# Optimization experiments

Hardware: AMD Instinct MI355X
Metric: run time of the kernel (lower is better)

The kernel has to match this reference:

```python
import jax, jax.numpy as jnp
import numpy as np

B, F, D = 1024, 160000, 16


def setup_inputs() -> dict:
    key = jax.random.key(0)
    k1, k2, k3 = jax.random.split(key, 3)
    x = jax.random.randint(k1, (B, F), 0, 2, dtype=jnp.int32)  # multi-hot transaction
    emb_w = jax.random.normal(k2, (F, D), dtype=jnp.float32) * 0.05  # FM factor table
    bias_w = jax.random.normal(k3, (F, 1), dtype=jnp.float32) * 0.05  # per-field linear bias
    g_bias = jnp.zeros((), dtype=jnp.float32)  # global bias
    return {"x": x, "emb_w": emb_w, "bias_w": bias_w, "g_bias": g_bias}


def reference(x, emb_w, bias_w, g_bias):
    # mask[b,f] = 1 where field f is active (row > 0 in original tf code)
    mask = (x > 0).astype(emb_w.dtype)  # [B, F]
    # sum of active embeddings per row: equals gather+sum in the original
    ev = mask @ emb_w  # [B, D]
    # sum of squared norms of active embeddings per row
    rowsq = jnp.sum(emb_w * emb_w, axis=1)  # [F]
    sum_sq = mask @ rowsq  # [B]
    # 0.5 * (sum_{i,j} e_i . e_j - sum_i ||e_i||^2) == FM pairwise interaction
    second = 0.5 * (jnp.sum(ev * ev, axis=-1) - sum_sq)  # [B]
    # linear term: global bias + sum of active field biases
    linear = g_bias + mask @ bias_w  # [B, 1]
    return linear + second[:, None]  # [B, 1]
```

## Files before the change

kernel.cpp:

```cpp
#include <hip/hip_runtime.h>

#define B_ROWS 1024
#define F_FLD  160000
#define D_DIM  16
#define TCOLS  256
#define NCHUNK (F_FLD / TCOLS)
#define NSTAT  (D_DIM + 1)
#define ACC_N  (B_ROWS * NSTAT)
#define RED_SLAB 25

__global__ __launch_bounds__(256) void fm_prep(const float* __restrict__ emb,
                                               const float* __restrict__ bias,
                                               float* __restrict__ c,
                                               float* __restrict__ acc) {
    int i = blockIdx.x * 256 + threadIdx.x;
    if (i < F_FLD) {
        const float4* e = (const float4*)(emb + (size_t)i * D_DIM);
        float4 e0 = e[0], e1 = e[1], e2 = e[2], e3 = e[3];
        float s = e0.x*e0.x + e0.y*e0.y + e0.z*e0.z + e0.w*e0.w
                + e1.x*e1.x + e1.y*e1.y + e1.z*e1.z + e1.w*e1.w
                + e2.x*e2.x + e2.y*e2.y + e2.z*e2.z + e2.w*e2.w
                + e3.x*e3.x + e3.y*e3.y + e3.z*e3.z + e3.w*e3.w;
        c[i] = bias[i] - 0.5f * s;
    }
    if (i < ACC_N) acc[i] = 0.0f;
}

__global__ __launch_bounds__(256) void fm_main(const int* __restrict__ x,
                                               const float* __restrict__ emb,
                                               const float* __restrict__ c,
                                               float* __restrict__ partial,
                                               float* __restrict__ acc,
                                               int use_partial) {
    __shared__ unsigned long long msk[4][256];
    const int tid  = threadIdx.x;
    const int wave = tid >> 6;
    const int lane = tid & 63;
    const int rowbase = blockIdx.y * 256;
    const int c0 = blockIdx.x * TCOLS;

    {
        const int4* xp = (const int4*)(x + (size_t)(rowbase + wave * 64) * F_FLD + c0)
                         + lane;
        const size_t rstride = F_FLD / 4;
        for (int i = 0; i < 64; i += 8) {
            int4 v[8];
#pragma unroll
            for (int k = 0; k < 8; ++k) v[k] = xp[(size_t)(i + k) * rstride];
#pragma unroll
            for (int k = 0; k < 8; ++k) {
                unsigned long long m0 = __ballot(v[k].x > 0);
                unsigned long long m1 = __ballot(v[k].y > 0);
                unsigned long long m2 = __ballot(v[k].z > 0);
                unsigned long long m3 = __ballot(v[k].w > 0);
                if (lane == 0) {
                    int r = wave * 64 + i + k;
                    msk[0][r] = m0; msk[1][r] = m1; msk[2][r] = m2; msk[3][r] = m3;
                }
            }
        }
    }
    __syncthreads();

    unsigned long long m0 = msk[0][tid], m1 = msk[1][tid],
                       m2 = msk[2][tid], m3 = msk[3][tid];
    float ev[D_DIM];
#pragma unroll
    for (int d = 0; d < D_DIM; ++d) ev[d] = 0.0f;
    float cacc = 0.0f;

    const float* eb = emb + (size_t)c0 * D_DIM;
    const float* cb = c + c0;
#pragma unroll 4
    for (int l = 0; l < 64; ++l) {
#pragma unroll
        for (int j = 0; j < 4; ++j) {
            float mm = (((j == 0 ? m0 : j == 1 ? m1 : j == 2 ? m2 : m3) >> l) & 1ull)
                           ? 1.0f : 0.0f;
            const float4* e = (const float4*)(eb + (size_t)(4 * l + j) * D_DIM);
            float4 e0 = e[0], e1 = e[1], e2 = e[2], e3 = e[3];
            ev[0]  += mm * e0.x;  ev[1]  += mm * e0.y;
            ev[2]  += mm * e0.z;  ev[3]  += mm * e0.w;
            ev[4]  += mm * e1.x;  ev[5]  += mm * e1.y;
            ev[6]  += mm * e1.z;  ev[7]  += mm * e1.w;
            ev[8]  += mm * e2.x;  ev[9]  += mm * e2.y;
            ev[10] += mm * e2.z;  ev[11] += mm * e2.w;
            ev[12] += mm * e3.x;  ev[13] += mm * e3.y;
            ev[14] += mm * e3.z;  ev[15] += mm * e3.w;
            cacc   += mm * cb[4 * l + j];
        }
    }

    const int row = rowbase + tid;
    if (use_partial) {
        float* p = partial + (size_t)blockIdx.x * ACC_N + row;
#pragma unroll
        for (int d = 0; d < D_DIM; ++d) p[d * B_ROWS] = ev[d];
        p[D_DIM * B_ROWS] = cacc;
    } else {
#pragma unroll
        for (int d = 0; d < D_DIM; ++d) atomicAdd(acc + d * B_ROWS + row, ev[d]);
        atomicAdd(acc + D_DIM * B_ROWS + row, cacc);
    }
}

__global__ __launch_bounds__(256) void fm_reduce(const float* __restrict__ partial,
                                                 float* __restrict__ acc) {
    int t = blockIdx.x * 256 + threadIdx.x;
    if (t >= ACC_N) return;
    const float* p = partial + (size_t)blockIdx.y * RED_SLAB * ACC_N + t;
    float s = 0.0f;
#pragma unroll 5
    for (int k = 0; k < RED_SLAB; ++k) s += p[(size_t)k * ACC_N];
    atomicAdd(acc + t, s);
}

__global__ __launch_bounds__(256) void fm_final(const float* __restrict__ acc,
                                                const float* __restrict__ g_bias,
                                                float* __restrict__ out) {
    int row = blockIdx.x * 256 + threadIdx.x;
    if (row >= B_ROWS) return;
    float s = 0.0f;
#pragma unroll
    for (int d = 0; d < D_DIM; ++d) {
        float v = acc[d * B_ROWS + row];
        s += v * v;
    }
    out[row] = g_bias[0] + acc[D_DIM * B_ROWS + row] + 0.5f * s;
}

extern "C" void kernel_launch(void* const* d_in, const int* in_sizes, int n_in,
                              void* d_out, int out_size, void* d_ws, size_t ws_size,
                              hipStream_t stream) {
    const int*   x      = (const int*)d_in[0];
    const float* emb_w  = (const float*)d_in[1];
    const float* bias_w = (const float*)d_in[2];
    const float* g_bias = (const float*)d_in[3];
    float*       out    = (float*)d_out;

    size_t c_bytes   = (size_t)F_FLD * sizeof(float);
    size_t acc_bytes = (size_t)ACC_N * sizeof(float);
    size_t par_bytes = (size_t)NCHUNK * ACC_N * sizeof(float);
    float* c       = (float*)d_ws;
    float* acc     = (float*)((char*)d_ws + c_bytes);
    float* partial = (float*)((char*)d_ws + c_bytes + acc_bytes);
    int use_partial = (ws_size >= c_bytes + acc_bytes + par_bytes) ? 1 : 0;

    fm_prep<<<dim3((F_FLD + 255) / 256), dim3(256), 0, stream>>>(emb_w, bias_w, c, acc);
    fm_main<<<dim3(NCHUNK, B_ROWS / 256), dim3(256), 0, stream>>>(
        x, emb_w, c, partial, acc, use_partial);
    if (use_partial)
        fm_reduce<<<dim3((ACC_N + 255) / 256, NCHUNK / RED_SLAB), dim3(256), 0, stream>>>(
            partial, acc);
    fm_final<<<dim3((B_ROWS + 255) / 256), dim3(256), 0, stream>>>(acc, g_bias, out);
}
```

Measured before the change: 930.0 us.

## Compute masked embedding sums with bf16 MFMA instead of scalar FMA loops

Replaces the per-thread scalar loop over 256 fields with bf16 16x16x32 MFMA instructions. Ballot bitmasks are expanded into bf16 0/1 A-fragments, and a new pack kernel converts the embedding table and the combined bias/square-norm vector into bf16 B-fragment layout. Partials and accumulators move to a row-major [row][17] layout to match the MFMA output. This is meant to remove the ALU-bound FMA work, which costs far more than streaming x. In exchange it adds an extra pack pass, drops the block barrier before the mask reads, and rounds the embeddings and c terms to bf16, which risks accuracy.

```diff
diff --git a/kernel.cpp b/kernel.cpp
--- a/kernel.cpp
+++ b/kernel.cpp
@@ -1,13 +1,32 @@
 #include <hip/hip_runtime.h>
+#include <hip/hip_bf16.h>
 
 #define B_ROWS 1024
 #define F_FLD  160000
 #define D_DIM  16
 #define TCOLS  256
 #define NCHUNK (F_FLD / TCOLS)
+#define NKB    (F_FLD / 32)
 #define NSTAT  (D_DIM + 1)
 #define ACC_N  (B_ROWS * NSTAT)
 #define RED_SLAB 25
+
+typedef __attribute__((ext_vector_type(8))) short bf16x8;
+typedef __attribute__((ext_vector_type(4))) float f32x4;
+
+static __device__ inline unsigned short f2bf(float x) {
+    __hip_bfloat16 h = __float2bfloat16(x);
+    union { __hip_bfloat16 h; unsigned short s; } u; u.h = h; return u.s;
+}
+
+static __device__ inline bf16x8 expand8(unsigned b) {
+    union { unsigned u[4]; bf16x8 v; } r;
+    r.u[0] = ((b        & 1u) * 0x3F80u) | (((b >> 1) & 1u) * 0x3F800000u);
+    r.u[1] = (((b >> 2) & 1u) * 0x3F80u) | (((b >> 3) & 1u) * 0x3F800000u);
+    r.u[2] = (((b >> 4) & 1u) * 0x3F80u) | (((b >> 5) & 1u) * 0x3F800000u);
+    r.u[3] = (((b >> 6) & 1u) * 0x3F80u) | (((b >> 7) & 1u) * 0x3F800000u);
+    return r.v;
+}
 
 __global__ __launch_bounds__(256) void fm_prep(const float* __restrict__ emb,
                                                const float* __restrict__ bias,
@@ -26,81 +45,108 @@
     if (i < ACC_N) acc[i] = 0.0f;
 }
 
+__global__ __launch_bounds__(256) void fm_pack(const float* __restrict__ emb,
+                                               const float* __restrict__ c,
+                                               unsigned short* __restrict__ embB,
+                                               unsigned short* __restrict__ cB2c) {
+    const int tid = threadIdx.x;
+    const int kb = blockIdx.x * 4 + (tid >> 6);
+    const int l = tid & 63, q = l >> 4, n = l & 15;
+    union { unsigned short s[8]; uint4 u; } v;
+#pragma unroll
+    for (int j = 0; j < 8; ++j) {
+        int f = kb * 32 + 4 * j + q;
+        v.s[j] = f2bf(emb[(size_t)f * D_DIM + n]);
+    }
+    *(uint4*)(embB + ((size_t)kb * 64 + l) * 8) = v.u;
+    if (n == 0) {
+        union { unsigned short s[8]; uint4 u; } w;
+#pragma unroll
+        for (int j = 0; j < 8; ++j) w.s[j] = f2bf(c[kb * 32 + 4 * j + q]);
+        *(uint4*)(cB2c + ((size_t)kb * 4 + q) * 8) = w.u;
+    }
+}
+
 __global__ __launch_bounds__(256) void fm_main(const int* __restrict__ x,
-                                               const float* __restrict__ emb,
-                                               const float* __restrict__ c,
+                                               const unsigned short* __restrict__ embB,
+                                               const unsigned short* __restrict__ cB2c,
                                                float* __restrict__ partial,
                                                float* __restrict__ acc,
                                                int use_partial) {
-    __shared__ unsigned long long msk[4][256];
-    const int tid  = threadIdx.x;
-    const int wave = tid >> 6;
-    const int lane = tid & 63;
+    __shared__ unsigned long long msk[256][4];
+    const int tid = threadIdx.x;
+    const int w = tid >> 6, l = tid & 63;
+    const int q = l >> 4, n = l & 15;
     const int rowbase = blockIdx.y * 256;
     const int c0 = blockIdx.x * TCOLS;
+    const int kb0 = blockIdx.x * 8;
 
     {
-        const int4* xp = (const int4*)(x + (size_t)(rowbase + wave * 64) * F_FLD + c0)
-                         + lane;
-        const size_t rstride = F_FLD / 4;
+        const int4* xp = (const int4*)(x + (size_t)(rowbase + w * 64) * F_FLD + c0) + l;
+        const size_t rstr = F_FLD / 4;
         for (int i = 0; i < 64; i += 8) {
             int4 v[8];
 #pragma unroll
-            for (int k = 0; k < 8; ++k) v[k] = xp[(size_t)(i + k) * rstride];
+            for (int k = 0; k < 8; ++k) v[k] = xp[(size_t)(i + k) * rstr];
 #pragma unroll
             for (int k = 0; k < 8; ++k) {
                 unsigned long long m0 = __ballot(v[k].x > 0);
                 unsigned long long m1 = __ballot(v[k].y > 0);
                 unsigned long long m2 = __ballot(v[k].z > 0);
                 unsigned long long m3 = __ballot(v[k].w > 0);
-                if (lane == 0) {
-                    int r = wave * 64 + i + k;
-                    msk[0][r] = m0; msk[1][r] = m1; msk[2][r] = m2; msk[3][r] = m3;
+                if (l == 0) {
+                    int r = w * 64 + i + k;
+                    msk[r][0] = m0; msk[r][1] = m1; msk[r][2] = m2; msk[r][3] = m3;
                 }
             }
         }
     }
-    __syncthreads();
-
-    unsigned long long m0 = msk[0][tid], m1 = msk[1][tid],
-                       m2 = msk[2][tid], m3 = msk[3][tid];
-    float ev[D_DIM];
-#pragma unroll
-    for (int d = 0; d < D_DIM; ++d) ev[d] = 0.0f;
-    float cacc = 0.0f;
-
-    const float* eb = emb + (size_t)c0 * D_DIM;
-    const float* cb = c + c0;
-#pragma unroll 4
-    for (int l = 0; l < 64; ++l) {
-#pragma unroll
-        for (int j = 0; j < 4; ++j) {
-            float mm = (((j == 0 ? m0 : j == 1 ? m1 : j == 2 ? m2 : m3) >> l) & 1ull)
-                           ? 1.0f : 0.0f;
-            const float4* e = (const float4*)(eb + (size_t)(4 * l + j) * D_DIM);
-            float4 e0 = e[0], e1 = e[1], e2 = e[2], e3 = e[3];
-            ev[0]  += mm * e0.x;  ev[1]  += mm * e0.y;
-            ev[2]  += mm * e0.z;  ev[3]  += mm * e0.w;
-            ev[4]  += mm * e1.x;  ev[5]  += mm * e1.y;
-            ev[6]  += mm * e1.z;  ev[7]  += mm * e1.w;
-            ev[8]  += mm * e2.x;  ev[9]  += mm * e2.y;
-            ev[10] += mm * e2.z;  ev[11] += mm * e2.w;
-            ev[12] += mm * e3.x;  ev[13] += mm * e3.y;
-            ev[14] += mm * e3.z;  ev[15] += mm * e3.w;
-            cacc   += mm * cb[4 * l + j];
+
+    unsigned long long wq[4];
+#pragma unroll
+    for (int mt = 0; mt < 4; ++mt) wq[mt] = msk[w * 64 + mt * 16 + n][q];
+
+    f32x4 aev[4], ac[4];
+#pragma unroll
+    for (int mt = 0; mt < 4; ++mt) {
+        aev[mt] = (f32x4){0.f, 0.f, 0.f, 0.f};
+        ac[mt]  = (f32x4){0.f, 0.f, 0.f, 0.f};
+    }
+
+    const uint4* eB = (const uint4*)embB;
+    const uint4* cB = (const uint4*)cB2c;
+#pragma unroll
+    for (int s = 0; s < 8; ++s) {
+        union { uint4 u; bf16x8 v; } Bf, Cf;
+        Bf.u = eB[(size_t)(kb0 + s) * 64 + l];
+        Cf.u = cB[(size_t)(kb0 + s) * 4 + q];
+#pragma unroll
+        for (int mt = 0; mt < 4; ++mt) {
+            unsigned b = (unsigned)(wq[mt] >> (8 * s)) & 0xFFu;
+            bf16x8 A = expand8(b);
+            aev[mt] = __builtin_amdgcn_mfma_f32_16x16x32_bf16(A, Bf.v, aev[mt], 0, 0, 0);
+            ac[mt]  = __builtin_amdgcn_mfma_f32_16x16x32_bf16(A, Cf.v, ac[mt], 0, 0, 0);
         }
     }
 
-    const int row = rowbase + tid;
-    if (use_partial) {
-        float* p = partial + (size_t)blockIdx.x * ACC_N + row;
-#pragma unroll
-        for (int d = 0; d < D_DIM; ++d) p[d * B_ROWS] = ev[d];
-        p[D_DIM * B_ROWS] = cacc;
-    } else {
-#pragma unroll
-        for (int d = 0; d < D_DIM; ++d) atomicAdd(acc + d * B_ROWS + row, ev[d]);
-        atomicAdd(acc + D_DIM * B_ROWS + row, cacc);
+    const int ch = blockIdx.x;
+#pragma unroll
+    for (int mt = 0; mt < 4; ++mt) {
+        int rowg = rowbase + w * 64 + mt * 16 + q * 4;
+        if (use_partial) {
+#pragma unroll
+            for (int r = 0; r < 4; ++r) {
+                float* p = partial + ((size_t)ch * B_ROWS + rowg + r) * NSTAT;
+                p[n] = aev[mt][r];
+                if (n == 0) p[16] = ac[mt][r];
+            }
+        } else {
+#pragma unroll
+            for (int r = 0; r < 4; ++r) {
+                atomicAdd(acc + (size_t)(rowg + r) * NSTAT + n, aev[mt][r]);
+                if (n == 0) atomicAdd(acc + (size_t)(rowg + r) * NSTAT + 16, ac[mt][r]);
+            }
+        }
     }
 }
 
@@ -120,13 +166,11 @@
                                                 float* __restrict__ out) {
     int row = blockIdx.x * 256 + threadIdx.x;
     if (row >= B_ROWS) return;
+    const float* a = acc + (size_t)row * NSTAT;
     float s = 0.0f;
 #pragma unroll
-    for (int d = 0; d < D_DIM; ++d) {
-        float v = acc[d * B_ROWS + row];
-        s += v * v;
-    }
-    out[row] = g_bias[0] + acc[D_DIM * B_ROWS + row] + 0.5f * s;
+    for (int d = 0; d < D_DIM; ++d) s += a[d] * a[d];
+    out[row] = g_bias[0] + a[16] + 0.5f * s;
 }
 
 extern "C" void kernel_launch(void* const* d_in, const int* in_sizes, int n_in,
@@ -138,17 +182,24 @@
     const float* g_bias = (const float*)d_in[3];
     float*       out    = (float*)d_out;
 
-    size_t c_bytes   = (size_t)F_FLD * sizeof(float);
-    size_t acc_bytes = (size_t)ACC_N * sizeof(float);
-    size_t par_bytes = (size_t)NCHUNK * ACC_N * sizeof(float);
-    float* c       = (float*)d_ws;
-    float* acc     = (float*)((char*)d_ws + c_bytes);
-    float* partial = (float*)((char*)d_ws + c_bytes + acc_bytes);
-    int use_partial = (ws_size >= c_bytes + acc_bytes + par_bytes) ? 1 : 0;
+    size_t off_c    = 0;
+    size_t off_acc  = off_c   + (size_t)F_FLD * 4;
+    size_t off_embB = off_acc + (size_t)ACC_N * 4;
+    size_t off_cB   = off_embB + (size_t)NKB * 64 * 8 * 2;
+    size_t off_par  = off_cB  + (size_t)NKB * 4 * 8 * 2;
+    size_t total    = off_par + (size_t)NCHUNK * B_ROWS * NSTAT * 4;
+
+    float*          c       = (float*)((char*)d_ws + off_c);
+    float*          acc     = (float*)((char*)d_ws + off_acc);
+    unsigned short* embB    = (unsigned short*)((char*)d_ws + off_embB);
+    unsigned short* cB2c    = (unsigned short*)((char*)d_ws + off_cB);
+    float*          partial = (float*)((char*)d_ws + off_par);
+    int use_partial = (ws_size >= total) ? 1 : 0;
 
     fm_prep<<<dim3((F_FLD + 255) / 256), dim3(256), 0, stream>>>(emb_w, bias_w, c, acc);
+    fm_pack<<<dim3(NKB / 4), dim3(256), 0, stream>>>(emb_w, c, embB, cB2c);
     fm_main<<<dim3(NCHUNK, B_ROWS / 256), dim3(256), 0, stream>>>(
-        x, emb_w, c, partial, acc, use_partial);
+        x, embB, cB2c, partial, acc, use_partial);
     if (use_partial)
         fm_reduce<<<dim3((ACC_N + 255) / 256, NCHUNK / RED_SLAB), dim3(256), 0, stream>>>(
             partial, acc);
```

Result: faster. 858.1 us (-7.7%).
